# Kernel tuning notes

Measured on AMD Instinct MI355X. Metric: run time of the kernel, lower is better.

The kernel has to match this reference:

```python
import jax, jax.numpy as jnp
import numpy as np

H = 1024
EPS = 1e-5
N_ENT = 1000
TOP_K = 5


def _ln(x, g, b):
    mu = jnp.mean(x, axis=-1, keepdims=True)
    var = jnp.mean((x - mu) ** 2, axis=-1, keepdims=True)
    return (x - mu) * jax.lax.rsqrt(var + EPS) * g + b


def _gelu(x):
    return jax.nn.gelu(x, approximate=False)  # torch nn.GELU default (erf)


def setup_inputs() -> dict:
    key = jax.random.key(0)
    ks = jax.random.split(key, 24)
    s = 0.02
    inp = {
        'hidden_states': jax.random.normal(ks[0], (8, 2048, H), jnp.float32),
        'entity_embeddings': jax.random.normal(ks[1], (N_ENT, H), jnp.float32) * 0.01,
        # entity_encoder: H -> 2H -> H -> LN
        'ee_w1': jax.random.normal(ks[2], (H, 2 * H), jnp.float32) * s,
        'ee_b1': jnp.zeros((2 * H,), jnp.float32),
        'ee_w2': jax.random.normal(ks[3], (2 * H, H), jnp.float32) * s,
        'ee_b2': jnp.zeros((H,), jnp.float32),
        'ee_g': jnp.ones((H,), jnp.float32),
        'ee_beta': jnp.zeros((H,), jnp.float32),
        # relation_encoder: H -> H -> H -> LN
        're_w1': jax.random.normal(ks[4], (H, H), jnp.float32) * s,
        're_b1': jnp.zeros((H,), jnp.float32),
        're_w2': jax.random.normal(ks[5], (H, H), jnp.float32) * s,
        're_b2': jnp.zeros((H,), jnp.float32),
        're_g': jnp.ones((H,), jnp.float32),
        're_beta': jnp.zeros((H,), jnp.float32),
        # reasoning_network: 3H -> 2H -> H -> LN
        'rn_w1': jax.random.normal(ks[6], (3 * H, 2 * H), jnp.float32) * s,
        'rn_b1': jnp.zeros((2 * H,), jnp.float32),
        'rn_w2': jax.random.normal(ks[7], (2 * H, H), jnp.float32) * s,
        'rn_b2': jnp.zeros((H,), jnp.float32),
        'rn_g': jnp.ones((H,), jnp.float32),
        'rn_beta': jnp.zeros((H,), jnp.float32),
        # validation_network: H -> H/2 -> 1 -> sigmoid
        'vn_w1': jax.random.normal(ks[8], (H, H // 2), jnp.float32) * s,
        'vn_b1': jnp.zeros((H // 2,), jnp.float32),
        'vn_w2': jax.random.normal(ks[9], (H // 2, 1), jnp.float32) * s,
        'vn_b2': jnp.zeros((1,), jnp.float32),
    }
    return inp


def reference(hidden_states, entity_embeddings,
              ee_w1, ee_b1, ee_w2, ee_b2, ee_g, ee_beta,
              re_w1, re_b1, re_w2, re_b2, re_g, re_beta,
              rn_w1, rn_b1, rn_w2, rn_b2, rn_g, rn_beta,
              vn_w1, vn_b1, vn_w2, vn_b2):
    # entity encoder over all tokens: [B,S,H]
    entity_features = _ln(_gelu(hidden_states @ ee_w1 + ee_b1) @ ee_w2 + ee_b2, ee_g, ee_beta)

    # query=None path: relation encoder on mean-pooled hidden states [B,H]
    pooled = jnp.mean(hidden_states, axis=1)
    relation_features = _ln(_gelu(pooled @ re_w1 + re_b1) @ re_w2 + re_b2, re_g, re_beta)
    query_features = relation_features

    # similarity + top-k entity retrieval
    entity_similarities = query_features @ entity_embeddings.T  # [B, N_ENT]
    top_values, top_indices = jax.lax.top_k(entity_similarities, TOP_K)
    retrieved_entities = entity_embeddings[top_indices]  # [B, K, H]

    # reasoning input: [mean retrieved entity | relation | mean context]
    entity_vec = jnp.mean(retrieved_entities, axis=1)  # [B,H]
    context_vec = jnp.mean(hidden_states, axis=1)      # [B,H]
    reasoning_in = jnp.concatenate([entity_vec, relation_features, context_vec], axis=-1)  # [B,3H]
    reasoning_output = _ln(_gelu(reasoning_in @ rn_w1 + rn_b1) @ rn_w2 + rn_b2, rn_g, rn_beta)

    validation_scores = jax.nn.sigmoid(_gelu(reasoning_output @ vn_w1 + vn_b1) @ vn_w2 + vn_b2)

    return (entity_features, relation_features, retrieved_entities,
            entity_similarities, top_indices, reasoning_output, validation_scores)
```

## Files before the change

kernel.cpp:

```cpp
#include <hip/hip_runtime.h>
#include <math.h>

#define H 1024
#define SEQ 2048
#define BATCH 8
#define N_ENT 1000
#define TOPK 5
#define LN_EPS 1e-5f

using bf16x8 = __attribute__((ext_vector_type(8))) __bf16;
using f32x4  = __attribute__((ext_vector_type(4))) float;
#define AS1 __attribute__((address_space(1)))
#define AS3 __attribute__((address_space(3)))


__device__ __forceinline__ float gelu_fast(float x) {
    float z = fabsf(x) * 0.70710678118654752440f;
    float t = __builtin_amdgcn_rcpf(fmaf(0.3275911f, z, 1.0f));
    float p = fmaf(fmaf(fmaf(fmaf(1.061405429f, t, -1.453152027f), t, 1.421413741f),
                        t, -0.284496736f), t, 0.254829592f) * t;
    float e = __builtin_amdgcn_exp2f(-z * z * 1.44269504088896f);
    float erfz = fmaf(-p, e, 1.0f);
    float s = copysignf(erfz, x);
    return 0.5f * x * (1.0f + s);
}

__device__ __forceinline__ float sigmoidf_(float x) {
    return 1.0f / (1.0f + expf(-x));
}

__device__ __forceinline__ unsigned short f2bf(float f) {
    unsigned int u = __float_as_uint(f);
    unsigned int r = (u + 0x7fffu + ((u >> 16) & 1u)) >> 16;
    return (unsigned short)r;
}

__device__ float block_sum(float v, float* red) {
    for (int off = 32; off > 0; off >>= 1) v += __shfl_down(v, off, 64);
    int wid = threadIdx.x >> 6;
    int lane = threadIdx.x & 63;
    int nw = blockDim.x >> 6;
    if (lane == 0) red[wid] = v;
    __syncthreads();
    if (threadIdx.x == 0) {
        float s = 0.f;
        for (int i = 0; i < nw; ++i) s += red[i];
        red[0] = s;
    }
    __syncthreads();
    float r = red[0];
    __syncthreads();
    return r;
}


__global__ void f2bf_kernel(const float* __restrict__ in, unsigned short* __restrict__ out, int n) {
    int i = (blockIdx.x * blockDim.x + threadIdx.x) * 4;
    if (i >= n) return;
    float4 v = *(const float4*)(in + i);
    ushort4 o;
    o.x = f2bf(v.x); o.y = f2bf(v.y); o.z = f2bf(v.z); o.w = f2bf(v.w);
    *(ushort4*)(out + i) = o;
}

__global__ void transpose_bf_kernel(const float* __restrict__ in, unsigned short* __restrict__ out,
                                    int R, int C) {
    __shared__ float tile[32][33];
    int c0 = blockIdx.x * 32, r0 = blockIdx.y * 32;
    int tx = threadIdx.x & 31, ty = threadIdx.x >> 5;
#pragma unroll
    for (int i = 0; i < 32; i += 8)
        tile[ty + i][tx] = in[(size_t)(r0 + ty + i) * C + c0 + tx];
    __syncthreads();
#pragma unroll
    for (int i = 0; i < 32; i += 8)
        out[(size_t)(c0 + ty + i) * R + r0 + tx] = f2bf(tile[tx][ty + i]);
}


__global__ void pool1_kernel(const float* __restrict__ hs, float* __restrict__ part,
                             unsigned short* __restrict__ hsb) {
    int sc = blockIdx.x, b = blockIdx.y, t = threadIdx.x;
    size_t rowbase = (size_t)b * SEQ + sc * 64;
    const float* p = hs + rowbase * H + t * 4;
    float4 a = {0.f, 0.f, 0.f, 0.f};
    for (int s = 0; s < 64; ++s) {
        float4 v = *(const float4*)(p + (size_t)s * H);
        a.x += v.x; a.y += v.y; a.z += v.z; a.w += v.w;
        if (hsb) {
            ushort4 o;
            o.x = f2bf(v.x); o.y = f2bf(v.y); o.z = f2bf(v.z); o.w = f2bf(v.w);
            *(ushort4*)(hsb + (rowbase + s) * H + t * 4) = o;
        }
    }
    *(float4*)(part + ((size_t)b * 32 + sc) * H + t * 4) = a;
}

__global__ void pool2_kernel(const float* __restrict__ part, float* __restrict__ pooled) {
    int b = blockIdx.x, t = threadIdx.x;
    float4 s = {0.f, 0.f, 0.f, 0.f};
    for (int sc = 0; sc < 32; ++sc) {
        float4 v = *(const float4*)(part + ((size_t)b * 32 + sc) * H + t * 4);
        s.x += v.x; s.y += v.y; s.z += v.z; s.w += v.w;
    }
    float4 o = {s.x * (1.0f / SEQ), s.y * (1.0f / SEQ), s.z * (1.0f / SEQ), s.w * (1.0f / SEQ)};
    *(float4*)(pooled + (size_t)b * H + t * 4) = o;
}


template <int KRANGE>
__global__ void mlp_partial_kernel(const float* __restrict__ X, int ldx,
                                   const float* __restrict__ W, int N,
                                   float* __restrict__ part) {
    __shared__ float xs[8][KRANGE];
    int jb = blockIdx.x, ks = blockIdx.y, t = threadIdx.x;
    int k0 = ks * KRANGE;
    for (int i = t; i < 8 * KRANGE; i += 256) {
        int b = i / KRANGE, k = i % KRANGE;
        xs[b][k] = X[(size_t)b * ldx + k0 + k];
    }
    __syncthreads();
    int j = jb * 256 + t;
    float acc[8] = {};
    for (int k = 0; k < KRANGE; ++k) {
        float w = W[(size_t)(k0 + k) * N + j];
#pragma unroll
        for (int b = 0; b < 8; ++b) acc[b] = fmaf(xs[b][k], w, acc[b]);
    }
#pragma unroll
    for (int b = 0; b < 8; ++b) part[((size_t)ks * 8 + b) * N + j] = acc[b];
}

__global__ void mlp_reduce_gelu_kernel(const float* __restrict__ part, const float* __restrict__ bias,
                                       float* __restrict__ out, int N, int nks) {
    int b = blockIdx.y;
    int j = blockIdx.x * 256 + threadIdx.x;
    float s = bias[j];
    for (int ks = 0; ks < nks; ++ks) s += part[((size_t)ks * 8 + b) * N + j];
    out[(size_t)b * N + j] = gelu_fast(s);
}

__global__ void mlp_reduce_ln_kernel(const float* __restrict__ part, const float* __restrict__ bias,
                                     const float* __restrict__ g, const float* __restrict__ be,
                                     float* __restrict__ out, int nks) {
    __shared__ float red[32];
    int b = blockIdx.x, t = threadIdx.x;
    float s = bias[t];
    for (int ks = 0; ks < nks; ++ks) s += part[((size_t)ks * 8 + b) * H + t];
    float mu = block_sum(s, red) * (1.0f / H);
    float d = s - mu;
    float var = block_sum(d * d, red) * (1.0f / H);
    out[(size_t)b * H + t] = d * rsqrtf(var + LN_EPS) * g[t] + be[t];
}


__global__ void sim_kernel(const float* __restrict__ rel, const float* __restrict__ ent,
                           float* __restrict__ sims) {
    __shared__ float rl[8 * H];
    int t = threadIdx.x;
    for (int i = t; i < 8 * H; i += 256) rl[i] = rel[i];
    __syncthreads();
    int e = blockIdx.x * 4 + (t >> 6);
    int lane = t & 63;
    float ev[16];
    const float* ep = ent + (size_t)e * H;
#pragma unroll
    for (int i = 0; i < 16; ++i) ev[i] = ep[lane + i * 64];
#pragma unroll
    for (int b = 0; b < 8; ++b) {
        float a = 0.f;
#pragma unroll
        for (int i = 0; i < 16; ++i) a = fmaf(ev[i], rl[b * H + lane + i * 64], a);
        for (int off = 32; off > 0; off >>= 1) a += __shfl_down(a, off, 64);
        if (lane == 0) sims[b * N_ENT + e] = a;
    }
}

__global__ void topk_kernel(const float* __restrict__ sims, float* __restrict__ out_idx_f,
                            int* __restrict__ idx_i) {
    __shared__ float v[1024];
    __shared__ float rv[4];
    __shared__ int ri[4];
    int b = blockIdx.x, t = threadIdx.x;
    for (int i = t; i < 1024; i += 256) v[i] = (i < N_ENT) ? sims[b * N_ENT + i] : -INFINITY;
    __syncthreads();
    for (int k = 0; k < TOPK; ++k) {
        float best = -INFINITY;
        int bi = 0x7fffffff;
        for (int i = t; i < 1024; i += 256) {
            float x = v[i];
            if (x > best || (x == best && i < bi)) { best = x; bi = i; }
        }
        for (int off = 32; off > 0; off >>= 1) {
            float ov = __shfl_down(best, off, 64);
            int oi = __shfl_down(bi, off, 64);
            if (ov > best || (ov == best && oi < bi)) { best = ov; bi = oi; }
        }
        if ((t & 63) == 0) { rv[t >> 6] = best; ri[t >> 6] = bi; }
        __syncthreads();
        if (t == 0) {
            for (int w = 1; w < 4; ++w)
                if (rv[w] > rv[0] || (rv[w] == rv[0] && ri[w] < ri[0])) { rv[0] = rv[w]; ri[0] = ri[w]; }
            int sel = ri[0];
            out_idx_f[b * TOPK + k] = (float)sel;
            idx_i[b * TOPK + k] = sel;
            v[sel] = -INFINITY;
        }
        __syncthreads();
    }
}

__global__ void gather_concat_kernel(const float* __restrict__ ent, const int* __restrict__ idx,
                                     const float* __restrict__ rel, const float* __restrict__ pooled,
                                     float* __restrict__ retrieved, float* __restrict__ xin) {
    int b = blockIdx.x, h = threadIdx.x;
    float acc = 0.f;
    for (int k = 0; k < TOPK; ++k) {
        float v = ent[(size_t)idx[b * TOPK + k] * H + h];
        retrieved[((size_t)b * TOPK + k) * H + h] = v;
        acc += v;
    }
    float* xb = xin + (size_t)b * 3 * H;
    xb[h] = acc * (1.0f / TOPK);
    xb[H + h] = rel[b * H + h];
    xb[2 * H + h] = pooled[b * H + h];
}

__global__ void vn_final_kernel(const float* __restrict__ part, const float* __restrict__ b1,
                                const float* __restrict__ w2, const float* __restrict__ b2,
                                float* __restrict__ vs, int nks) {
    __shared__ float red[32];
    int b = blockIdx.x, t = threadIdx.x;
    float s = b1[t];
    for (int ks = 0; ks < nks; ++ks) s += part[((size_t)ks * 8 + b) * 512 + t];
    float c = gelu_fast(s) * w2[t];
    float tot = block_sum(c, red);
    if (t == 0) vs[b] = sigmoidf_(tot + b2[0]);
}

template <int GELU_BF16_OUT>
__global__ __launch_bounds__(256) void gemm_mfma(const unsigned short* __restrict__ A,
                                                 const unsigned short* __restrict__ Bt,
                                                 const float* __restrict__ bias,
                                                 void* __restrict__ Cout,
                                                 int M, int N, int K) {
    __shared__ __align__(16) unsigned short As[2][128 * 32];
    __shared__ __align__(16) unsigned short Bs[2][128 * 32];
    const int tid = threadIdx.x;
    const int lane = tid & 63;

    const int Mp = M >> 7, Np = N >> 7;
    const int GM = 8;
    int per_group = GM * Np;
    int group = blockIdx.x / per_group;
    int rem = blockIdx.x - group * per_group;
    int gbase = group * GM;
    int gm = Mp - gbase; if (gm > GM) gm = GM;
    const int m0 = (gbase + rem % gm) * 128;
    const int n0 = (rem / gm) * 128;

    const int wave = tid >> 6;
    const int wm = (wave >> 1) * 64, wn = (wave & 1) * 64;
    const int rowA_f = wm + (lane & 15);
    const int rowB_f = wn + (lane & 15);
    const int kq = (lane >> 4) * 8;

    auto stage = [&](int kbase, int buf) {
#pragma unroll
        for (int r = 0; r < 2; ++r) {
            int e = (r * 256 + tid) * 8;
            int row = e >> 5, kk = e & 31;
            const unsigned short* ga = A + (size_t)(m0 + row) * K + kbase + kk;
            const unsigned short* gb = Bt + (size_t)(n0 + row) * K + kbase + kk;
            unsigned short* la = &As[buf][(size_t)(r * 256 + (tid & ~63)) * 8];
            unsigned short* lb = &Bs[buf][(size_t)(r * 256 + (tid & ~63)) * 8];
            __builtin_amdgcn_global_load_lds((AS1 void*)ga, (AS3 void*)la, 16, 0, 0);
            __builtin_amdgcn_global_load_lds((AS1 void*)gb, (AS3 void*)lb, 16, 0, 0);
        }
    };

    f32x4 acc[4][4] = {};
    stage(0, 0);
    int cur = 0;
    for (int k0 = 0; k0 < K; k0 += 32) {
        __syncthreads();
        if (k0 + 32 < K) stage(k0 + 32, cur ^ 1);
        const unsigned short* Ab = As[cur];
        const unsigned short* Bb = Bs[cur];
        bf16x8 af[4], bfg[4];
#pragma unroll
        for (int i = 0; i < 4; ++i)
            af[i] = *(const bf16x8*)(Ab + (rowA_f + i * 16) * 32 + kq);
#pragma unroll
        for (int j = 0; j < 4; ++j)
            bfg[j] = *(const bf16x8*)(Bb + (rowB_f + j * 16) * 32 + kq);
#pragma unroll
        for (int i = 0; i < 4; ++i)
#pragma unroll
            for (int j = 0; j < 4; ++j)
                acc[i][j] = __builtin_amdgcn_mfma_f32_16x16x32_bf16(af[i], bfg[j], acc[i][j], 0, 0, 0);
        cur ^= 1;
    }

    const int cn = lane & 15;
    const int rbase = (lane >> 4) * 4;
#pragma unroll
    for (int i = 0; i < 4; ++i) {
#pragma unroll
        for (int j = 0; j < 4; ++j) {
            int n = n0 + wn + j * 16 + cn;
            float bv = bias[n];
            int mb = m0 + wm + i * 16 + rbase;
#pragma unroll
            for (int r = 0; r < 4; ++r) {
                float c = acc[i][j][r] + bv;
                if (GELU_BF16_OUT) {
                    c = gelu_fast(c);
                    ((unsigned short*)Cout)[(size_t)(mb + r) * N + n] = f2bf(c);
                } else {
                    ((float*)Cout)[(size_t)(mb + r) * N + n] = c;
                }
            }
        }
    }
}

__global__ void ln_rows_kernel(float* __restrict__ x, const float* __restrict__ g,
                               const float* __restrict__ beta) {
    __shared__ float red[32];
    float* p = x + (size_t)blockIdx.x * H;
    int t = threadIdx.x;
    float4 v = *(const float4*)(p + t * 4);
    float s = v.x + v.y + v.z + v.w;
    float mu = block_sum(s, red) * (1.0f / H);
    float4 d = { v.x - mu, v.y - mu, v.z - mu, v.w - mu };
    float d2 = d.x * d.x + d.y * d.y + d.z * d.z + d.w * d.w;
    float var = block_sum(d2, red) * (1.0f / H);
    float inv = rsqrtf(var + LN_EPS);
    float4 gg = *(const float4*)(g + t * 4);
    float4 bb = *(const float4*)(beta + t * 4);
    float4 o = { d.x * inv * gg.x + bb.x, d.y * inv * gg.y + bb.y,
                 d.z * inv * gg.z + bb.z, d.w * inv * gg.w + bb.w };
    *(float4*)(p + t * 4) = o;
}


extern "C" void kernel_launch(void* const* d_in, const int* in_sizes, int n_in,
                              void* d_out, int out_size, void* d_ws, size_t ws_size,
                              hipStream_t stream) {
    const float* hs     = (const float*)d_in[0];
    const float* ent    = (const float*)d_in[1];
    const float* ee_w1  = (const float*)d_in[2];
    const float* ee_b1  = (const float*)d_in[3];
    const float* ee_w2  = (const float*)d_in[4];
    const float* ee_b2  = (const float*)d_in[5];
    const float* ee_g   = (const float*)d_in[6];
    const float* ee_be  = (const float*)d_in[7];
    const float* re_w1  = (const float*)d_in[8];
    const float* re_b1  = (const float*)d_in[9];
    const float* re_w2  = (const float*)d_in[10];
    const float* re_b2  = (const float*)d_in[11];
    const float* re_g   = (const float*)d_in[12];
    const float* re_be  = (const float*)d_in[13];
    const float* rn_w1  = (const float*)d_in[14];
    const float* rn_b1  = (const float*)d_in[15];
    const float* rn_w2  = (const float*)d_in[16];
    const float* rn_b2  = (const float*)d_in[17];
    const float* rn_g   = (const float*)d_in[18];
    const float* rn_be  = (const float*)d_in[19];
    const float* vn_w1  = (const float*)d_in[20];
    const float* vn_b1  = (const float*)d_in[21];
    const float* vn_w2  = (const float*)d_in[22];
    const float* vn_b2  = (const float*)d_in[23];

    float* out = (float*)d_out;
    float* ef   = out;
    float* rel  = ef + (size_t)BATCH * SEQ * H;
    float* retr = rel + BATCH * H;
    float* sims = retr + BATCH * TOPK * H;
    float* tidx = sims + BATCH * N_ENT;
    float* ro   = tidx + BATCH * TOPK;
    float* vs   = ro + BATCH * H;

    float* ws = (float*)d_ws;
    size_t o = 0;
    float* pooled = ws + o; o += 8192;
    int*   idx_i  = (int*)(ws + o); o += 64;
    float* xin    = ws + o; o += 8 * 3 * H;
    float* h1r    = ws + o; o += 8 * H;
    float* h1n    = ws + o; o += 8 * 2 * H;
    float* part   = ws + o; o += 24 * 8 * 2048;
    unsigned short* w1t = (unsigned short*)(ws + o); o += (2048 * 1024) / 2;
    unsigned short* w2t = (unsigned short*)(ws + o); o += (2048 * 1024) / 2;
    unsigned short* hsb = (unsigned short*)(ws + o);

    long long avail = (long long)(ws_size / 4) - (long long)o;
    int chunk = (int)(avail / 1536);
    chunk &= ~127;
    int total = BATCH * SEQ;
    if (chunk > total) chunk = total;
    if (chunk < 128) chunk = 128;
    bool full = (chunk >= total);
    unsigned short* midb = hsb + (size_t)chunk * H;

    transpose_bf_kernel<<<dim3(2048 / 32, 1024 / 32), 256, 0, stream>>>(ee_w1, w1t, 1024, 2048);
    transpose_bf_kernel<<<dim3(1024 / 32, 2048 / 32), 256, 0, stream>>>(ee_w2, w2t, 2048, 1024);

    pool1_kernel<<<dim3(32, BATCH), 256, 0, stream>>>(hs, part, full ? hsb : nullptr);
    pool2_kernel<<<BATCH, 256, 0, stream>>>(part, pooled);

    mlp_partial_kernel<64><<<dim3(4, 16), 256, 0, stream>>>(pooled, H, re_w1, H, part);
    mlp_reduce_gelu_kernel<<<dim3(4, 8), 256, 0, stream>>>(part, re_b1, h1r, H, 16);
    mlp_partial_kernel<64><<<dim3(4, 16), 256, 0, stream>>>(h1r, H, re_w2, H, part);
    mlp_reduce_ln_kernel<<<BATCH, 1024, 0, stream>>>(part, re_b2, re_g, re_be, rel, 16);

    sim_kernel<<<250, 256, 0, stream>>>(rel, ent, sims);
    topk_kernel<<<BATCH, 256, 0, stream>>>(sims, tidx, idx_i);
    gather_concat_kernel<<<BATCH, 1024, 0, stream>>>(ent, idx_i, rel, pooled, retr, xin);

    mlp_partial_kernel<128><<<dim3(8, 24), 256, 0, stream>>>(xin, 3 * H, rn_w1, 2 * H, part);
    mlp_reduce_gelu_kernel<<<dim3(8, 8), 256, 0, stream>>>(part, rn_b1, h1n, 2 * H, 24);
    mlp_partial_kernel<128><<<dim3(4, 16), 256, 0, stream>>>(h1n, 2 * H, rn_w2, H, part);
    mlp_reduce_ln_kernel<<<BATCH, 1024, 0, stream>>>(part, rn_b2, rn_g, rn_be, ro, 16);

    mlp_partial_kernel<128><<<dim3(2, 8), 256, 0, stream>>>(ro, H, vn_w1, 512, part);
    vn_final_kernel<<<BATCH, 512, 0, stream>>>(part, vn_b1, vn_w2, vn_b2, vs, 8);

    for (int r0 = 0; r0 < total; r0 += chunk) {
        int m = total - r0;
        if (m > chunk) m = chunk;
        if (!full) {
            int nconv = m * H;
            f2bf_kernel<<<(nconv / 4 + 255) / 256, 256, 0, stream>>>(hs + (size_t)r0 * H, hsb, nconv);
        }
        unsigned short* a1 = full ? (hsb + (size_t)r0 * H) : hsb;
        gemm_mfma<1><<<(m / 128) * (2048 / 128), 256, 0, stream>>>(a1, w1t, ee_b1, midb,
                                                                   m, 2048, 1024);
        gemm_mfma<0><<<(m / 128) * (1024 / 128), 256, 0, stream>>>(midb, w2t, ee_b2,
                                                                   ef + (size_t)r0 * H,
                                                                   m, 1024, 2048);
    }
    ln_rows_kernel<<<total, 256, 0, stream>>>(ef, ee_g, ee_be);
}
```

Before: 577.6 us.

## Replace 128x128 MFMA GEMM with 256x256 tile, 8-wave, 4-slot pipelined kernel

Replaces the entity-encoder GEMM with a 256x256 tile, 512-thread kernel. It uses BK=64 and a four-slot LDS ring staged in half-tiles, with XOR-swizzled LDS addressing to avoid bank conflicts. The K loop is split into four MFMA phases, each interleaved with async global-to-LDS loads, explicit vmcnt waits, barriers and s_setprio. The aim is more data reuse per tile and better overlap of loads with MFMA work. The larger tile cuts grid size (fewer workgroups for the 16K-row GEMMs), raises register and LDS pressure, and requires chunk sizes to be multiples of 256.

```diff
diff --git a/kernel.cpp b/kernel.cpp
--- a/kernel.cpp
+++ b/kernel.cpp
@@ -239,86 +239,179 @@
 }
 
 template <int GELU_BF16_OUT>
-__global__ __launch_bounds__(256) void gemm_mfma(const unsigned short* __restrict__ A,
-                                                 const unsigned short* __restrict__ Bt,
-                                                 const float* __restrict__ bias,
-                                                 void* __restrict__ Cout,
-                                                 int M, int N, int K) {
-    __shared__ __align__(16) unsigned short As[2][128 * 32];
-    __shared__ __align__(16) unsigned short Bs[2][128 * 32];
+__global__ __launch_bounds__(512, 2) void gemm256_8ph(const unsigned short* __restrict__ A,
+                                                      const unsigned short* __restrict__ Bt,
+                                                      const float* __restrict__ bias,
+                                                      void* __restrict__ Cout,
+                                                      int M, int N, int K) {
+    __shared__ __align__(16) unsigned short As[4][128 * 64];
+    __shared__ __align__(16) unsigned short Bs[4][128 * 64];
     const int tid = threadIdx.x;
     const int lane = tid & 63;
-
-    const int Mp = M >> 7, Np = N >> 7;
-    const int GM = 8;
-    int per_group = GM * Np;
-    int group = blockIdx.x / per_group;
-    int rem = blockIdx.x - group * per_group;
-    int gbase = group * GM;
-    int gm = Mp - gbase; if (gm > GM) gm = GM;
-    const int m0 = (gbase + rem % gm) * 128;
-    const int n0 = (rem / gm) * 128;
-
-    const int wave = tid >> 6;
-    const int wm = (wave >> 1) * 64, wn = (wave & 1) * 64;
-    const int rowA_f = wm + (lane & 15);
-    const int rowB_f = wn + (lane & 15);
-    const int kq = (lane >> 4) * 8;
-
-    auto stage = [&](int kbase, int buf) {
-#pragma unroll
-        for (int r = 0; r < 2; ++r) {
-            int e = (r * 256 + tid) * 8;
-            int row = e >> 5, kk = e & 31;
-            const unsigned short* ga = A + (size_t)(m0 + row) * K + kbase + kk;
-            const unsigned short* gb = Bt + (size_t)(n0 + row) * K + kbase + kk;
-            unsigned short* la = &As[buf][(size_t)(r * 256 + (tid & ~63)) * 8];
-            unsigned short* lb = &Bs[buf][(size_t)(r * 256 + (tid & ~63)) * 8];
-            __builtin_amdgcn_global_load_lds((AS1 void*)ga, (AS3 void*)la, 16, 0, 0);
-            __builtin_amdgcn_global_load_lds((AS1 void*)gb, (AS3 void*)lb, 16, 0, 0);
-        }
+    const int w = tid >> 6;
+    const int wm2 = w >> 2;
+    const int wn4 = w & 3;
+
+    const int Np = N >> 8;
+    const int nwg = gridDim.x;
+    int bid = blockIdx.x;
+    int s = bid;
+    if ((nwg & 7) == 0) s = (bid & 7) * (nwg >> 3) + (bid >> 3);
+    const int m0 = (s / Np) << 8;
+    const int n0 = (s % Np) << 8;
+
+    const int nT = K >> 6;
+
+    const int l7 = lane & 7;
+    const int lrow0 = w * 16 + (lane >> 3);
+    const int lrow1 = lrow0 + 8;
+    const int kel0 = ((l7 ^ (lrow0 & 7)) << 3);
+    const int kel1 = ((l7 ^ (lrow1 & 7)) << 3);
+    const unsigned short* pa0 = A + (size_t)(m0 + lrow0) * K + kel0;
+    const unsigned short* pa1 = A + (size_t)(m0 + lrow1) * K + kel1;
+    const unsigned short* pb0 = Bt + (size_t)(n0 + lrow0) * K + kel0;
+    const unsigned short* pb1 = Bt + (size_t)(n0 + lrow1) * K + kel1;
+    const size_t halfstep = (size_t)128 * K;
+    const int dst0 = (w * 16) * 64;
+    const int dst1 = dst0 + 8 * 64;
+
+    auto stageA = [&](int t, int half) {
+        if (t >= nT) return;
+        int slot = (2 * t + half) & 3;
+        int koff = t << 6;
+        __builtin_amdgcn_global_load_lds((AS1 void*)(pa0 + half * halfstep + koff),
+                                         (AS3 void*)(&As[slot][dst0]), 16, 0, 0);
+        __builtin_amdgcn_global_load_lds((AS1 void*)(pa1 + half * halfstep + koff),
+                                         (AS3 void*)(&As[slot][dst1]), 16, 0, 0);
     };
-
-    f32x4 acc[4][4] = {};
-    stage(0, 0);
-    int cur = 0;
-    for (int k0 = 0; k0 < K; k0 += 32) {
-        __syncthreads();
-        if (k0 + 32 < K) stage(k0 + 32, cur ^ 1);
-        const unsigned short* Ab = As[cur];
-        const unsigned short* Bb = Bs[cur];
-        bf16x8 af[4], bfg[4];
-#pragma unroll
-        for (int i = 0; i < 4; ++i)
-            af[i] = *(const bf16x8*)(Ab + (rowA_f + i * 16) * 32 + kq);
-#pragma unroll
-        for (int j = 0; j < 4; ++j)
-            bfg[j] = *(const bf16x8*)(Bb + (rowB_f + j * 16) * 32 + kq);
-#pragma unroll
-        for (int i = 0; i < 4; ++i)
-#pragma unroll
-            for (int j = 0; j < 4; ++j)
-                acc[i][j] = __builtin_amdgcn_mfma_f32_16x16x32_bf16(af[i], bfg[j], acc[i][j], 0, 0, 0);
-        cur ^= 1;
+    auto stageB = [&](int t, int half) {
+        if (t >= nT) return;
+        int slot = (2 * t + half) & 3;
+        int koff = t << 6;
+        __builtin_amdgcn_global_load_lds((AS1 void*)(pb0 + half * halfstep + koff),
+                                         (AS3 void*)(&Bs[slot][dst0]), 16, 0, 0);
+        __builtin_amdgcn_global_load_lds((AS1 void*)(pb1 + half * halfstep + koff),
+                                         (AS3 void*)(&Bs[slot][dst1]), 16, 0, 0);
+    };
+
+    const int arow = lane & 15;
+    const int xk0 = (((lane >> 4) << 4)) ^ (l7 << 4);
+    const int xk1 = (64 + ((lane >> 4) << 4)) ^ (l7 << 4);
+    auto ldf = [&](const unsigned short* slotbase, int rowbase, int xk) -> bf16x8 {
+        return *(const bf16x8*)((const char*)slotbase + (rowbase + arow) * 128 + xk);
+    };
+
+    f32x4 acc[8][4] = {};
+
+    stageA(0, 0); stageA(0, 1); stageB(0, 0); stageB(0, 1);
+    asm volatile("s_waitcnt vmcnt(4)" ::: "memory");
+    stageA(1, 0); stageB(1, 0); stageB(1, 1);
+    asm volatile("s_waitcnt vmcnt(6)" ::: "memory");
+    __builtin_amdgcn_s_barrier();
+
+    bf16x8 af0[4][2], af1[4][2], bf0[2][2], bf1[2][2];
+
+    for (int T = 0; T < nT; ++T) {
+        const unsigned short* Aslot0 = As[(2 * T) & 3];
+        const unsigned short* Aslot1 = As[(2 * T + 1) & 3];
+        const unsigned short* Bslot0 = Bs[(2 * T) & 3];
+        const unsigned short* Bslot1 = Bs[(2 * T + 1) & 3];
+
+#pragma unroll
+        for (int ii = 0; ii < 4; ++ii) {
+            af0[ii][0] = ldf(Aslot0, ii * 32 + wm2 * 16, xk0);
+            af0[ii][1] = ldf(Aslot0, ii * 32 + wm2 * 16, xk1);
+        }
+#pragma unroll
+        for (int jj = 0; jj < 2; ++jj) {
+            bf0[jj][0] = ldf(Bslot0, jj * 64 + wn4 * 16, xk0);
+            bf0[jj][1] = ldf(Bslot0, jj * 64 + wn4 * 16, xk1);
+        }
+        stageA(T + 1, 1);
+        __builtin_amdgcn_s_barrier();
+        __builtin_amdgcn_s_setprio(1);
+#pragma unroll
+        for (int ii = 0; ii < 4; ++ii)
+#pragma unroll
+            for (int jj = 0; jj < 2; ++jj) {
+                acc[ii][jj] = __builtin_amdgcn_mfma_f32_16x16x32_bf16(af0[ii][0], bf0[jj][0], acc[ii][jj], 0, 0, 0);
+                acc[ii][jj] = __builtin_amdgcn_mfma_f32_16x16x32_bf16(af0[ii][1], bf0[jj][1], acc[ii][jj], 0, 0, 0);
+            }
+        __builtin_amdgcn_s_setprio(0);
+        __builtin_amdgcn_s_barrier();
+
+#pragma unroll
+        for (int jj = 0; jj < 2; ++jj) {
+            bf1[jj][0] = ldf(Bslot1, jj * 64 + wn4 * 16, xk0);
+            bf1[jj][1] = ldf(Bslot1, jj * 64 + wn4 * 16, xk1);
+        }
+        stageA(T + 2, 0);
+        __builtin_amdgcn_s_barrier();
+        __builtin_amdgcn_s_setprio(1);
+#pragma unroll
+        for (int ii = 0; ii < 4; ++ii)
+#pragma unroll
+            for (int jj = 0; jj < 2; ++jj) {
+                acc[ii][2 + jj] = __builtin_amdgcn_mfma_f32_16x16x32_bf16(af0[ii][0], bf1[jj][0], acc[ii][2 + jj], 0, 0, 0);
+                acc[ii][2 + jj] = __builtin_amdgcn_mfma_f32_16x16x32_bf16(af0[ii][1], bf1[jj][1], acc[ii][2 + jj], 0, 0, 0);
+            }
+        __builtin_amdgcn_s_setprio(0);
+        __builtin_amdgcn_s_barrier();
+
+#pragma unroll
+        for (int ii = 0; ii < 4; ++ii) {
+            af1[ii][0] = ldf(Aslot1, ii * 32 + wm2 * 16, xk0);
+            af1[ii][1] = ldf(Aslot1, ii * 32 + wm2 * 16, xk1);
+        }
+        stageB(T + 2, 0);
+        __builtin_amdgcn_s_barrier();
+        __builtin_amdgcn_s_setprio(1);
+#pragma unroll
+        for (int ii = 0; ii < 4; ++ii)
+#pragma unroll
+            for (int jj = 0; jj < 2; ++jj) {
+                acc[4 + ii][jj] = __builtin_amdgcn_mfma_f32_16x16x32_bf16(af1[ii][0], bf0[jj][0], acc[4 + ii][jj], 0, 0, 0);
+                acc[4 + ii][jj] = __builtin_amdgcn_mfma_f32_16x16x32_bf16(af1[ii][1], bf0[jj][1], acc[4 + ii][jj], 0, 0, 0);
+            }
+        __builtin_amdgcn_s_setprio(0);
+        __builtin_amdgcn_s_barrier();
+
+        stageB(T + 2, 1);
+        if (T + 3 <= nT) {
+            asm volatile("s_waitcnt vmcnt(6)" ::: "memory");
+        } else {
+            asm volatile("s_waitcnt vmcnt(0)" ::: "memory");
+        }
+        __builtin_amdgcn_s_barrier();
+        __builtin_amdgcn_s_setprio(1);
+#pragma unroll
+        for (int ii = 0; ii < 4; ++ii)
+#pragma unroll
+            for (int jj = 0; jj < 2; ++jj) {
+                acc[4 + ii][2 + jj] = __builtin_amdgcn_mfma_f32_16x16x32_bf16(af1[ii][0], bf1[jj][0], acc[4 + ii][2 + jj], 0, 0, 0);
+                acc[4 + ii][2 + jj] = __builtin_amdgcn_mfma_f32_16x16x32_bf16(af1[ii][1], bf1[jj][1], acc[4 + ii][2 + jj], 0, 0, 0);
+            }
+        __builtin_amdgcn_s_setprio(0);
+        __builtin_amdgcn_s_barrier();
     }
 
     const int cn = lane & 15;
     const int rbase = (lane >> 4) * 4;
 #pragma unroll
-    for (int i = 0; i < 4; ++i) {
+    for (int i = 0; i < 8; ++i) {
+        int mbase = m0 + (i >> 2) * 128 + (i & 3) * 32 + wm2 * 16 + rbase;
 #pragma unroll
         for (int j = 0; j < 4; ++j) {
-            int n = n0 + wn + j * 16 + cn;
+            int n = n0 + (j >> 1) * 128 + (j & 1) * 64 + wn4 * 16 + cn;
             float bv = bias[n];
-            int mb = m0 + wm + i * 16 + rbase;
 #pragma unroll
             for (int r = 0; r < 4; ++r) {
                 float c = acc[i][j][r] + bv;
                 if (GELU_BF16_OUT) {
                     c = gelu_fast(c);
-                    ((unsigned short*)Cout)[(size_t)(mb + r) * N + n] = f2bf(c);
+                    ((unsigned short*)Cout)[(size_t)(mbase + r) * N + n] = f2bf(c);
                 } else {
-                    ((float*)Cout)[(size_t)(mb + r) * N + n] = c;
+                    ((float*)Cout)[(size_t)(mbase + r) * N + n] = c;
                 }
             }
         }
@@ -396,10 +489,10 @@
 
     long long avail = (long long)(ws_size / 4) - (long long)o;
     int chunk = (int)(avail / 1536);
-    chunk &= ~127;
+    chunk &= ~255;
     int total = BATCH * SEQ;
     if (chunk > total) chunk = total;
-    if (chunk < 128) chunk = 128;
+    if (chunk < 256) chunk = 256;
     bool full = (chunk >= total);
     unsigned short* midb = hsb + (size_t)chunk * H;
 
@@ -434,11 +527,11 @@
             f2bf_kernel<<<(nconv / 4 + 255) / 256, 256, 0, stream>>>(hs + (size_t)r0 * H, hsb, nconv);
         }
         unsigned short* a1 = full ? (hsb + (size_t)r0 * H) : hsb;
-        gemm_mfma<1><<<(m / 128) * (2048 / 128), 256, 0, stream>>>(a1, w1t, ee_b1, midb,
-                                                                   m, 2048, 1024);
-        gemm_mfma<0><<<(m / 128) * (1024 / 128), 256, 0, stream>>>(midb, w2t, ee_b2,
-                                                                   ef + (size_t)r0 * H,
-                                                                   m, 1024, 2048);
+        gemm256_8ph<1><<<(m / 256) * (2048 / 256), 512, 0, stream>>>(a1, w1t, ee_b1, midb,
+                                                                     m, 2048, 1024);
+        gemm256_8ph<0><<<(m / 256) * (1024 / 256), 512, 0, stream>>>(midb, w2t, ee_b2,
+                                                                     ef + (size_t)r0 * H,
+                                                                     m, 1024, 2048);
     }
     ln_rows_kernel<<<total, 256, 0, stream>>>(ef, ee_g, ee_be);
 }
```

Result: faster. 537.1 us (-7.0%).
